# Kernel optimization log

Hardware: AMD Instinct MI355X
Metric: run time of the kernel (lower is better)

## Reference

```python
import jax, jax.numpy as jnp
import numpy as np

B, C4, N, L4 = 8, 64, 512, 12
CQ = C4 // 4  # conv output channels


def setup_inputs() -> dict:
    key = jax.random.key(0)
    k_x, k_wc, k_bc, k_wg, k_bg = jax.random.split(key, 5)
    x = jax.random.normal(k_x, (B, C4, N, L4), dtype=jnp.float32)
    # Conv2d(in_dim, in_dim//4, kernel_size=(1,1)) -> pointwise: weight (CQ, C4)
    W_conv = jax.random.normal(k_wc, (CQ, C4), dtype=jnp.float32) / np.sqrt(C4)
    b_conv = jax.random.normal(k_bc, (CQ,), dtype=jnp.float32) * 0.01
    # Linear(in_dim, in_dim)
    W_gcn = jax.random.normal(k_wg, (C4, C4), dtype=jnp.float32) / np.sqrt(C4)
    b_gcn = jax.random.normal(k_bg, (C4,), dtype=jnp.float32) * 0.01
    return {"x": x, "W_conv": W_conv, "b_conv": b_conv, "W_gcn": W_gcn, "b_gcn": b_gcn}


def reference(x, W_conv, b_conv, W_gcn, b_gcn):
    # --- SpatioTemporalCorrelationComputation ---
    # 1x1 conv over channels: (b,c4,n,l) -> (b,cq,n,l)
    Fc = jnp.einsum('oc,bcnl->bonl', W_conv, x) + b_conv[None, :, None, None]
    Fl = Fc[:, :, :, -1]                                   # b,cq,n (last time step)
    xy = jnp.einsum('bcn,bcmt->bnmt', Fl, Fc)              # b,n,n,l4
    xx = jnp.sqrt(jnp.einsum('bcn,bcn->bc', Fl, Fl))       # b,cq
    yy = jnp.sqrt(jnp.einsum('bcnt,bcnt->bc', Fc, Fc))     # b,cq
    l2 = jnp.einsum('bc,bc->b', xx, yy)[:, None, None, None]
    S = xy / l2                                            # b,n,n,l4

    # --- RelationalFeatureExtraction ---
    # Loop-based R[:, :, :, k] = sum_j S[:,k,None,:,j] * F4[:,:,:,j]
    # is exactly this single contraction (Se expansion never materialized):
    R = jnp.einsum('bknj,bcnj->bcnk', S, x)                # b,c4,n,n

    # --- GraphOperation ---
    A = jax.nn.relu(jnp.tanh(jnp.max(R, axis=1)))          # b,n,n
    xg = jnp.einsum('bcnk,bkn->bck', R, A)                 # b,c4,n
    # Linear over channel dim: Fg[b,o,k] = sum_c xg[b,c,k] W[o,c] + bias[o]
    Fg = jnp.einsum('bck,oc->bok', xg, W_gcn) + b_gcn[None, :, None]
    return Fg[..., None]                                   # b,c4,n,1
```

## Files before the change

kernel.cpp:

```cpp
#include <hip/hip_runtime.h>
#include <hip/hip_bf16.h>
#include <math.h>

#define B    8
#define C4   64
#define CQ   16
#define NN   512
#define L4   12
#define XSP  100

#define O_TH   0
#define O_TL   (O_TH + (size_t)B*1024*NN/2)
#define O_T2H  (O_TL + (size_t)B*1024*NN/2)
#define O_T2L  (O_T2H + (size_t)B*NN*1024/2)
#define O_FL   (O_T2L + (size_t)B*NN*1024/2)
#define O_XX   (O_FL + (size_t)B*CQ*NN)
#define O_YY   (O_XX + B*CQ)
#define O_AH   (O_YY + B*CQ)
#define O_AL   (O_AH + (size_t)B*NN*NN/2)
#define O_FCG  (O_AL + (size_t)B*NN*NN/2)

typedef __attribute__((ext_vector_type(8))) short short8;
typedef __attribute__((ext_vector_type(4))) float floatx4;
typedef __attribute__((ext_vector_type(16))) float floatx16;

__device__ inline void split2(float x0, float x1, uint& hw, uint& lw) {
  uint u0 = __float_as_uint(x0), u1 = __float_as_uint(x1);
  uint h0 = u0 >> 16, h1 = u1 >> 16;
  float r0 = x0 - __uint_as_float(h0 << 16);
  float r1 = x1 - __uint_as_float(h1 << 16);
  hw = h0 | (h1 << 16);
  lw = (__float_as_uint(r0) >> 16) | ((__float_as_uint(r1) >> 16) << 16);
}

__global__ __launch_bounds__(256) void k1a_fc(const float* __restrict__ x,
                                              const float* __restrict__ Wc,
                                              const float* __restrict__ bc,
                                              float* __restrict__ ws) {
  int id = blockIdx.x;
  int b = id & 7;
  int nch = id >> 3;
  int n0 = nch * 8;
  int t = threadIdx.x;
  __shared__ __align__(16) float xs[C4*XSP];
  __shared__ float wcs[CQ*65];
  __shared__ float bcs[CQ];
  __shared__ __align__(16) float fcs[8*CQ*L4];

  for (int e = t; e < CQ*C4; e += 256) {
    int q = e >> 6, c = e & 63;
    wcs[q*65 + c] = Wc[e];
  }
  if (t < CQ) bcs[t] = bc[t];
  const float* xb = x + (size_t)b*C4*NN*L4 + (size_t)n0*L4;
  for (int f = t; f < C4*24; f += 256) {
    int c = f / 24, r = f - c*24;
    float4 v = *(const float4*)(xb + (size_t)c*NN*L4 + r*4);
    *(float4*)(xs + c*XSP + r*4) = v;
  }
  __syncthreads();
  {
    int q = t & 15, slot = t >> 4;
    float accv[6];
    #pragma unroll
    for (int i = 0; i < 6; ++i) accv[i] = bcs[q];
    for (int c = 0; c < C4; ++c) {
      float wv = wcs[q*65 + c];
      const float* xc = xs + c*XSP;
      #pragma unroll
      for (int i = 0; i < 6; ++i) accv[i] += wv * xc[slot + 16*i];
    }
    #pragma unroll
    for (int i = 0; i < 6; ++i) {
      int nj = slot + 16*i;
      int nl = nj / L4, j = nj - nl*L4;
      fcs[nl*(CQ*L4) + q*L4 + j] = accv[i];
      if (j == L4-1) ws[O_FL + ((size_t)b*CQ + q)*NN + n0 + nl] = accv[i];
    }
  }
  __syncthreads();
  if (t < CQ) {
    float yy = 0.f, xx = 0.f;
    for (int nl = 0; nl < 8; ++nl) {
      #pragma unroll
      for (int j = 0; j < L4; ++j) { float v = fcs[nl*(CQ*L4) + t*L4 + j]; yy += v*v; }
      float w = fcs[nl*(CQ*L4) + t*L4 + (L4-1)];
      xx += w*w;
    }
    atomicAdd(ws + O_YY + b*CQ + t, yy);
    atomicAdd(ws + O_XX + b*CQ + t, xx);
  }
  float* fcg = ws + O_FCG + (size_t)(b*64 + nch)*1536;
  for (int f = t; f < 384; f += 256)
    *(float4*)(fcg + f*4) = *(const float4*)(fcs + f*4);
}

__global__ __launch_bounds__(256, 4) void k1t_T(const float* __restrict__ x,
                                                float* __restrict__ ws) {
  int id = blockIdx.x;
  int b = id & 7;
  int nch = id >> 3;
  int n0 = nch * 8;
  int t = threadIdx.x;
  __shared__ __align__(16) float xs[C4*XSP];
  __shared__ __align__(16) float fcs[8*CQ*L4];
  const float* xb = x + (size_t)b*C4*NN*L4 + (size_t)n0*L4;
  for (int f = t; f < C4*24; f += 256) {
    int c = f / 24, r = f - c*24;
    float4 v = *(const float4*)(xb + (size_t)c*NN*L4 + r*4);
    *(float4*)(xs + c*XSP + r*4) = v;
  }
  {
    const float* fcg = ws + O_FCG + (size_t)(b*64 + nch)*1536;
    for (int f = t; f < 384; f += 256)
      *(float4*)(fcs + f*4) = *(const float4*)(fcg + f*4);
  }
  __syncthreads();
  int c = t >> 2, q0 = (t & 3) * 4;
  float vals[4][8];
  ushort* T2H = (ushort*)(ws + O_T2H);
  ushort* T2L = (ushort*)(ws + O_T2L);
  for (int nl = 0; nl < 8; ++nl) {
    float xr[L4];
    *(float4*)&xr[0] = *(const float4*)(xs + c*XSP + nl*L4);
    *(float4*)&xr[4] = *(const float4*)(xs + c*XSP + nl*L4 + 4);
    *(float4*)&xr[8] = *(const float4*)(xs + c*XSP + nl*L4 + 8);
    float tvp[4];
    #pragma unroll
    for (int i = 0; i < 4; ++i) {
      const float* fq = fcs + nl*(CQ*L4) + (q0+i)*L4;
      float a = 0.f;
      #pragma unroll
      for (int j = 0; j < L4; ++j) a += fq[j] * xr[j];
      tvp[i] = a;
      vals[i][nl] = a;
    }
    uint hw0, lw0, hw1, lw1;
    split2(tvp[0], tvp[1], hw0, lw0);
    split2(tvp[2], tvp[3], hw1, lw1);
    size_t off2 = ((size_t)b*NN + n0 + nl)*1024 + t*4;
    *(uint2*)(T2H + off2) = make_uint2(hw0, hw1);
    *(uint2*)(T2L + off2) = make_uint2(lw0, lw1);
  }
  ushort* TH = (ushort*)(ws + O_TH);
  ushort* TL = (ushort*)(ws + O_TL);
  #pragma unroll
  for (int i = 0; i < 4; ++i) {
    int m = c*16 + q0 + i;
    uint hw[4], lw[4];
    #pragma unroll
    for (int jj = 0; jj < 4; ++jj)
      split2(vals[i][2*jj], vals[i][2*jj+1], hw[jj], lw[jj]);
    size_t off = ((size_t)b*1024 + m)*NN + n0;
    *(uint4*)(TH + off) = make_uint4(hw[0], hw[1], hw[2], hw[3]);
    *(uint4*)(TL + off) = make_uint4(lw[0], lw[1], lw[2], lw[3]);
  }
}

__global__ __launch_bounds__(256, 4) void k2_mfma(float* __restrict__ ws) {
  int id = blockIdx.x;
  int b = id & 7;
  int rest = id >> 3;
  int kh = rest & 1;
  int nch = rest >> 1;
  int t = threadIdx.x;
  int w = t >> 6, lane = t & 63;
  int col = lane & 31, half = lane >> 5;

  __shared__ float l2tmp[CQ];
  if (t < CQ) l2tmp[t] = sqrtf(ws[O_XX + b*CQ + t]) * sqrtf(ws[O_YY + b*CQ + t]);
  __syncthreads();
  float l2sum = 0.f;
  #pragma unroll
  for (int q = 0; q < CQ; ++q) l2sum += l2tmp[q];
  float l2inv = 1.0f / l2sum;

  const float* flb = ws + O_FL + (size_t)b*CQ*NN;
  short8 bhf[2], blf[2];
  int kcol[2];
  #pragma unroll
  for (int kt = 0; kt < 2; ++kt) {
    kcol[kt] = kh*256 + w*64 + kt*32 + col;
    float f[8];
    #pragma unroll
    for (int e = 0; e < 8; ++e) f[e] = flb[(size_t)(half*8 + e)*NN + kcol[kt]];
    #pragma unroll
    for (int p = 0; p < 4; ++p) {
      uint hw, lw;
      split2(f[2*p], f[2*p+1], hw, lw);
      ((uint*)&bhf[kt])[p] = hw;
      ((uint*)&blf[kt])[p] = lw;
    }
  }
  const ushort* T2H = (const ushort*)(ws + O_T2H) + ((size_t)b*NN + nch*8)*1024;
  const ushort* T2L = (const ushort*)(ws + O_T2L) + ((size_t)b*NN + nch*8)*1024;
  ushort* AH = (ushort*)(ws + O_AH) + ((size_t)b*NN + nch*8)*NN;
  ushort* AL = (ushort*)(ws + O_AL) + ((size_t)b*NN + nch*8)*NN;

  for (int i = 0; i < 8; ++i) {
    short8 ah[2], al[2];
    #pragma unroll
    for (int ct = 0; ct < 2; ++ct) {
      size_t off = (size_t)i*1024 + (ct*32 + col)*16 + half*8;
      ah[ct] = *(const short8*)(T2H + off);
      al[ct] = *(const short8*)(T2L + off);
    }
    floatx16 acc[2][2];
    #pragma unroll
    for (int ct = 0; ct < 2; ++ct)
      #pragma unroll
      for (int kt = 0; kt < 2; ++kt) {
        floatx16 a = {0.f,0.f,0.f,0.f,0.f,0.f,0.f,0.f,
                      0.f,0.f,0.f,0.f,0.f,0.f,0.f,0.f};
        a = __builtin_amdgcn_mfma_f32_32x32x16_bf16(ah[ct], bhf[kt], a, 0, 0, 0);
        a = __builtin_amdgcn_mfma_f32_32x32x16_bf16(ah[ct], blf[kt], a, 0, 0, 0);
        a = __builtin_amdgcn_mfma_f32_32x32x16_bf16(al[ct], bhf[kt], a, 0, 0, 0);
        acc[ct][kt] = a;
      }
    #pragma unroll
    for (int kt = 0; kt < 2; ++kt) {
      float m = acc[0][kt][0];
      #pragma unroll
      for (int ct = 0; ct < 2; ++ct)
        #pragma unroll
        for (int rg = 0; rg < 16; ++rg)
          if (ct + rg) m = fmaxf(m, acc[ct][kt][rg]);
      m = fmaxf(m, __shfl_xor(m, 32));
      float xp = fmaxf(m * l2inv, 0.f);
      float av = 1.f - __fdividef(2.f, __expf(2.f * xp) + 1.f);
      uint u = __float_as_uint(av);
      uint hh = u >> 16;
      float r = av - __uint_as_float(hh << 16);
      ushort lv = (ushort)(__float_as_uint(r) >> 16);
      if (half == 0) {
        AH[(size_t)i*NN + kcol[kt]] = (ushort)hh;
        AL[(size_t)i*NN + kcol[kt]] = lv;
      }
    }
  }
}

__global__ __launch_bounds__(256, 2) void k3_mfma(const float* __restrict__ Wg,
                                                  const float* __restrict__ bg,
                                                  float* __restrict__ ws,
                                                  float* __restrict__ out) {
  int id = blockIdx.x;
  int b = id & 7;
  int rest = id >> 3;
  int kb = rest & 7;
  int mbb = rest >> 3;
  int t = threadIdx.x;
  int lane = t & 63;
  int w = t >> 6;
  int mw = w >> 1, kw = w & 1;
  int row = lane & 15, quad = lane >> 4;

  __shared__ __align__(16) ushort Ah[128*32];
  __shared__ __align__(16) ushort Al[128*32];
  __shared__ __align__(16) ushort Bh[64*32];
  __shared__ __align__(16) ushort Bl[64*32];
  __shared__ float l2tmp[CQ];
  __shared__ float wgs[C4*8];
  __shared__ float xg_s[8][64];

  if (t < CQ) l2tmp[t] = sqrtf(ws[O_XX + b*CQ + t]) * sqrtf(ws[O_YY + b*CQ + t]);
  for (int e = t; e < C4*8; e += 256) {
    int o = e >> 3, cl = e & 7;
    wgs[e] = Wg[o*C4 + mbb*8 + cl];
  }

  const ushort* TH = (const ushort*)(ws + O_TH) + ((size_t)b*1024 + mbb*128)*NN;
  const ushort* TL = (const ushort*)(ws + O_TL) + ((size_t)b*1024 + mbb*128)*NN;
  const ushort* AHp = (const ushort*)(ws + O_AH) + ((size_t)b*NN + kb*64)*NN;
  const ushort* ALp = (const ushort*)(ws + O_AL) + ((size_t)b*NN + kb*64)*NN;

  floatx4 acc[4][2];
  #pragma unroll
  for (int i = 0; i < 4; ++i)
    #pragma unroll
    for (int j = 0; j < 2; ++j) acc[i][j] = (floatx4){0.f, 0.f, 0.f, 0.f};

  for (int ksx = 0; ksx < 16; ++ksx) {
    int p0 = ksx*32;
    __syncthreads();
    #pragma unroll
    for (int i = 0; i < 2; ++i) {
      int f = t + 256*i;
      int m = f >> 2, seg = (f & 3) * 8;
      *(uint4*)(Ah + m*32 + seg) = *(const uint4*)(TH + (size_t)m*NN + p0 + seg);
      *(uint4*)(Al + m*32 + seg) = *(const uint4*)(TL + (size_t)m*NN + p0 + seg);
    }
    {
      int j = t >> 2, seg = (t & 3) * 8;
      *(uint4*)(Bh + j*32 + seg) = *(const uint4*)(AHp + (size_t)j*NN + p0 + seg);
      *(uint4*)(Bl + j*32 + seg) = *(const uint4*)(ALp + (size_t)j*NN + p0 + seg);
    }
    __syncthreads();
    short8 bh[2], bl[2];
    #pragma unroll
    for (int kt = 0; kt < 2; ++kt) {
      int jrow = kw*32 + kt*16 + row;
      bh[kt] = *(const short8*)(Bh + jrow*32 + quad*8);
      bl[kt] = *(const short8*)(Bl + jrow*32 + quad*8);
    }
    #pragma unroll
    for (int mt = 0; mt < 4; ++mt) {
      int mrow = mw*64 + mt*16 + row;
      short8 ah = *(const short8*)(Ah + mrow*32 + quad*8);
      short8 al = *(const short8*)(Al + mrow*32 + quad*8);
      #pragma unroll
      for (int kt = 0; kt < 2; ++kt) {
        acc[mt][kt] = __builtin_amdgcn_mfma_f32_16x16x32_bf16(ah, bh[kt], acc[mt][kt], 0, 0, 0);
        acc[mt][kt] = __builtin_amdgcn_mfma_f32_16x16x32_bf16(ah, bl[kt], acc[mt][kt], 0, 0, 0);
        acc[mt][kt] = __builtin_amdgcn_mfma_f32_16x16x32_bf16(al, bh[kt], acc[mt][kt], 0, 0, 0);
      }
    }
  }
  float l2sum = 0.f;
  #pragma unroll
  for (int q = 0; q < CQ; ++q) l2sum += l2tmp[q];
  float l2inv = 1.0f / l2sum;

  const float* flb = ws + O_FL + (size_t)b*CQ*NN;
  float fl[2][4];
  #pragma unroll
  for (int kt = 0; kt < 2; ++kt) {
    int kcol = kb*64 + kw*32 + kt*16 + row;
    #pragma unroll
    for (int rg = 0; rg < 4; ++rg)
      fl[kt][rg] = flb[(size_t)(quad*4 + rg)*NN + kcol];
  }
  #pragma unroll
  for (int mt = 0; mt < 4; ++mt) {
    #pragma unroll
    for (int kt = 0; kt < 2; ++kt) {
      float s = fl[kt][0]*acc[mt][kt][0] + fl[kt][1]*acc[mt][kt][1]
              + fl[kt][2]*acc[mt][kt][2] + fl[kt][3]*acc[mt][kt][3];
      s += __shfl_xor(s, 32);
      s += __shfl_xor(s, 16);
      if (quad == 0)
        xg_s[mw*4 + mt][kw*32 + kt*16 + row] = s * l2inv;
    }
  }
  __syncthreads();
  int kl = t & 63, og = t >> 6;
  #pragma unroll
  for (int oi = 0; oi < 16; ++oi) {
    int o = og*16 + oi;
    float a = 0.f;
    #pragma unroll
    for (int cl = 0; cl < 8; ++cl) a += wgs[o*8 + cl] * xg_s[cl][kl];
    if (mbb == 0) a += bg[o];
    atomicAdd(out + ((size_t)(b*C4 + o))*NN + kb*64 + kl, a);
  }
}

extern "C" void kernel_launch(void* const* d_in, const int* in_sizes, int n_in,
                              void* d_out, int out_size, void* d_ws, size_t ws_size,
                              hipStream_t stream) {
  const float* x  = (const float*)d_in[0];
  const float* Wc = (const float*)d_in[1];
  const float* bc = (const float*)d_in[2];
  const float* Wg = (const float*)d_in[3];
  const float* bg = (const float*)d_in[4];
  float* ws  = (float*)d_ws;
  float* out = (float*)d_out;

  hipMemsetAsync(ws + O_XX, 0, 2*B*CQ*sizeof(float), stream);
  hipMemsetAsync(out, 0, (size_t)out_size, stream);

  k1a_fc <<<B*64,  256, 0, stream>>>(x, Wc, bc, ws);
  k1t_T  <<<B*64,  256, 0, stream>>>(x, ws);
  k2_mfma<<<B*128, 256, 0, stream>>>(ws);
  k3_mfma<<<B*64,  256, 0, stream>>>(Wg, bg, ws, out);
}
```

Before: 146.1 us.

## Fuse T2 producer and adjacency MFMA kernel, keeping T2 in shared memory

Merges the k1t_T kernel, which built the T2 hi/lo bf16 split tensors, with the k2_mfma kernel that consumes them to compute the max-over-channels adjacency. T2 now stays in LDS, so its global write and read-back disappear along with one kernel launch. Each block now covers all 512 k columns with four kt tiles per wave, where before two blocks split the columns. The cost is half as many blocks in the adjacency phase, more LDS per block (launch bounds lowered to 2) and more registers per thread.

```diff
diff --git a/kernel.cpp b/kernel.cpp
--- a/kernel.cpp
+++ b/kernel.cpp
@@ -11,9 +11,7 @@
 
 #define O_TH   0
 #define O_TL   (O_TH + (size_t)B*1024*NN/2)
-#define O_T2H  (O_TL + (size_t)B*1024*NN/2)
-#define O_T2L  (O_T2H + (size_t)B*NN*1024/2)
-#define O_FL   (O_T2L + (size_t)B*NN*1024/2)
+#define O_FL   (O_TL + (size_t)B*1024*NN/2)
 #define O_XX   (O_FL + (size_t)B*CQ*NN)
 #define O_YY   (O_XX + B*CQ)
 #define O_AH   (O_YY + B*CQ)
@@ -95,8 +93,8 @@
     *(float4*)(fcg + f*4) = *(const float4*)(fcs + f*4);
 }
 
-__global__ __launch_bounds__(256, 4) void k1t_T(const float* __restrict__ x,
-                                                float* __restrict__ ws) {
+__global__ __launch_bounds__(256, 2) void k12_TS(const float* __restrict__ x,
+                                                 float* __restrict__ ws) {
   int id = blockIdx.x;
   int b = id & 7;
   int nch = id >> 3;
@@ -104,6 +102,10 @@
   int t = threadIdx.x;
   __shared__ __align__(16) float xs[C4*XSP];
   __shared__ __align__(16) float fcs[8*CQ*L4];
+  __shared__ __align__(16) ushort t2h[8*1024];
+  __shared__ __align__(16) ushort t2l[8*1024];
+  __shared__ float l2tmp[CQ];
+
   const float* xb = x + (size_t)b*C4*NN*L4 + (size_t)n0*L4;
   for (int f = t; f < C4*24; f += 256) {
     int c = f / 24, r = f - c*24;
@@ -115,11 +117,11 @@
     for (int f = t; f < 384; f += 256)
       *(float4*)(fcs + f*4) = *(const float4*)(fcg + f*4);
   }
-  __syncthreads();
+  if (t < CQ) l2tmp[t] = sqrtf(ws[O_XX + b*CQ + t]) * sqrtf(ws[O_YY + b*CQ + t]);
+  __syncthreads();
+
   int c = t >> 2, q0 = (t & 3) * 4;
   float vals[4][8];
-  ushort* T2H = (ushort*)(ws + O_T2H);
-  ushort* T2L = (ushort*)(ws + O_T2L);
   for (int nl = 0; nl < 8; ++nl) {
     float xr[L4];
     *(float4*)&xr[0] = *(const float4*)(xs + c*XSP + nl*L4);
@@ -138,9 +140,8 @@
     uint hw0, lw0, hw1, lw1;
     split2(tvp[0], tvp[1], hw0, lw0);
     split2(tvp[2], tvp[3], hw1, lw1);
-    size_t off2 = ((size_t)b*NN + n0 + nl)*1024 + t*4;
-    *(uint2*)(T2H + off2) = make_uint2(hw0, hw1);
-    *(uint2*)(T2L + off2) = make_uint2(lw0, lw1);
+    *(uint2*)(t2h + nl*1024 + t*4) = make_uint2(hw0, hw1);
+    *(uint2*)(t2l + nl*1024 + t*4) = make_uint2(lw0, lw1);
   }
   ushort* TH = (ushort*)(ws + O_TH);
   ushort* TL = (ushort*)(ws + O_TL);
@@ -155,32 +156,21 @@
     *(uint4*)(TH + off) = make_uint4(hw[0], hw[1], hw[2], hw[3]);
     *(uint4*)(TL + off) = make_uint4(lw[0], lw[1], lw[2], lw[3]);
   }
-}
-
-__global__ __launch_bounds__(256, 4) void k2_mfma(float* __restrict__ ws) {
-  int id = blockIdx.x;
-  int b = id & 7;
-  int rest = id >> 3;
-  int kh = rest & 1;
-  int nch = rest >> 1;
-  int t = threadIdx.x;
+  __syncthreads();
+
+  float l2sum = 0.f;
+  #pragma unroll
+  for (int q = 0; q < CQ; ++q) l2sum += l2tmp[q];
+  float l2inv = 1.0f / l2sum;
+
   int w = t >> 6, lane = t & 63;
   int col = lane & 31, half = lane >> 5;
-
-  __shared__ float l2tmp[CQ];
-  if (t < CQ) l2tmp[t] = sqrtf(ws[O_XX + b*CQ + t]) * sqrtf(ws[O_YY + b*CQ + t]);
-  __syncthreads();
-  float l2sum = 0.f;
-  #pragma unroll
-  for (int q = 0; q < CQ; ++q) l2sum += l2tmp[q];
-  float l2inv = 1.0f / l2sum;
-
   const float* flb = ws + O_FL + (size_t)b*CQ*NN;
-  short8 bhf[2], blf[2];
-  int kcol[2];
-  #pragma unroll
-  for (int kt = 0; kt < 2; ++kt) {
-    kcol[kt] = kh*256 + w*64 + kt*32 + col;
+  short8 bhf[4], blf[4];
+  int kcol[4];
+  #pragma unroll
+  for (int kt = 0; kt < 4; ++kt) {
+    kcol[kt] = w*128 + kt*32 + col;
     float f[8];
     #pragma unroll
     for (int e = 0; e < 8; ++e) f[e] = flb[(size_t)(half*8 + e)*NN + kcol[kt]];
@@ -192,39 +182,35 @@
       ((uint*)&blf[kt])[p] = lw;
     }
   }
-  const ushort* T2H = (const ushort*)(ws + O_T2H) + ((size_t)b*NN + nch*8)*1024;
-  const ushort* T2L = (const ushort*)(ws + O_T2L) + ((size_t)b*NN + nch*8)*1024;
-  ushort* AH = (ushort*)(ws + O_AH) + ((size_t)b*NN + nch*8)*NN;
-  ushort* AL = (ushort*)(ws + O_AL) + ((size_t)b*NN + nch*8)*NN;
+  ushort* AH = (ushort*)(ws + O_AH) + ((size_t)b*NN + n0)*NN;
+  ushort* AL = (ushort*)(ws + O_AL) + ((size_t)b*NN + n0)*NN;
 
   for (int i = 0; i < 8; ++i) {
     short8 ah[2], al[2];
     #pragma unroll
     for (int ct = 0; ct < 2; ++ct) {
-      size_t off = (size_t)i*1024 + (ct*32 + col)*16 + half*8;
-      ah[ct] = *(const short8*)(T2H + off);
-      al[ct] = *(const short8*)(T2L + off);
-    }
-    floatx16 acc[2][2];
-    #pragma unroll
-    for (int ct = 0; ct < 2; ++ct)
-      #pragma unroll
-      for (int kt = 0; kt < 2; ++kt) {
+      int off = i*1024 + (ct*32 + col)*16 + half*8;
+      ah[ct] = *(const short8*)(t2h + off);
+      al[ct] = *(const short8*)(t2l + off);
+    }
+    #pragma unroll
+    for (int kt = 0; kt < 4; ++kt) {
+      floatx16 acc[2];
+      #pragma unroll
+      for (int ct = 0; ct < 2; ++ct) {
         floatx16 a = {0.f,0.f,0.f,0.f,0.f,0.f,0.f,0.f,
                       0.f,0.f,0.f,0.f,0.f,0.f,0.f,0.f};
         a = __builtin_amdgcn_mfma_f32_32x32x16_bf16(ah[ct], bhf[kt], a, 0, 0, 0);
         a = __builtin_amdgcn_mfma_f32_32x32x16_bf16(ah[ct], blf[kt], a, 0, 0, 0);
         a = __builtin_amdgcn_mfma_f32_32x32x16_bf16(al[ct], bhf[kt], a, 0, 0, 0);
-        acc[ct][kt] = a;
+        acc[ct] = a;
       }
-    #pragma unroll
-    for (int kt = 0; kt < 2; ++kt) {
-      float m = acc[0][kt][0];
+      float m = acc[0][0];
       #pragma unroll
       for (int ct = 0; ct < 2; ++ct)
         #pragma unroll
         for (int rg = 0; rg < 16; ++rg)
-          if (ct + rg) m = fmaxf(m, acc[ct][kt][rg]);
+          if (ct + rg) m = fmaxf(m, acc[ct][rg]);
       m = fmaxf(m, __shfl_xor(m, 32));
       float xp = fmaxf(m * l2inv, 0.f);
       float av = 1.f - __fdividef(2.f, __expf(2.f * xp) + 1.f);
@@ -370,7 +356,6 @@
   hipMemsetAsync(out, 0, (size_t)out_size, stream);
 
   k1a_fc <<<B*64,  256, 0, stream>>>(x, Wc, bc, ws);
-  k1t_T  <<<B*64,  256, 0, stream>>>(x, ws);
-  k2_mfma<<<B*128, 256, 0, stream>>>(ws);
+  k12_TS <<<B*64,  256, 0, stream>>>(x, ws);
   k3_mfma<<<B*64,  256, 0, stream>>>(Wg, bg, ws, out);
 }
```

Result: faster. 140.6 us (-3.8%).
